# Kernel tuning notes

Hardware: AMD Instinct MI355X
Metric: run time of the kernel (lower is better)

The kernel has to match this reference:

```python
import jax, jax.numpy as jnp
import numpy as np

B, C, H, W = 8, 512, 32, 32
NUM_HEADS = 8
HEAD_DIM = C // NUM_HEADS
SCALE = 1.0 / float(np.sqrt(HEAD_DIM))


def setup_inputs() -> dict:
    key = jax.random.key(0)
    ks = jax.random.split(key, 6)
    x = jax.random.normal(ks[0], (B, C, H, W), dtype=jnp.float32)
    attn_mask = jax.random.randint(ks[1], (B, H, W), 0, 2).astype(jnp.bool_)
    # 1x1 conv weights are equivalent to channel matmuls: (out_ch, in_ch)
    w_std = 1.0 / float(np.sqrt(C))
    qkv_w = jax.random.uniform(ks[2], (3 * C, C), jnp.float32, -w_std, w_std)
    qkv_b = jax.random.uniform(ks[3], (3 * C,), jnp.float32, -w_std, w_std)
    proj_w = jax.random.uniform(ks[4], (C, C), jnp.float32, -w_std, w_std)
    proj_b = jax.random.uniform(ks[5], (C,), jnp.float32, -w_std, w_std)
    return {"x": x, "attn_mask": attn_mask, "qkv_w": qkv_w, "qkv_b": qkv_b,
            "proj_w": proj_w, "proj_b": proj_b}


def reference(x, attn_mask, qkv_w, qkv_b, proj_w, proj_b):
    b, c, h, w = x.shape
    S = h * w
    neg = jnp.finfo(x.dtype).min
    # qkv 1x1 conv: (B,3C,H,W)
    qkv = jnp.einsum('oc,bchw->bohw', qkv_w, x) + qkv_b[None, :, None, None]
    q, k, v = jnp.split(qkv, 3, axis=1)

    def split_heads(z):
        # (B, C, H, W) -> (B, heads, head_dim, S)
        return z.reshape(b, NUM_HEADS, HEAD_DIM, S)

    q, k, v = split_heads(q), split_heads(k), split_heads(v)
    # scores[s,t] = sum_d q[d,s] * k[d,t]
    scores = jnp.einsum('bhds,bhdt->bhst', q, k) * SCALE
    idx = jnp.arange(S)
    causal = (idx[None, :] > idx[:, None])[None, None]  # (1,1,S,S), True above diag
    scores = jnp.where(causal, neg, scores)
    kpm = attn_mask.reshape(b, 1, 1, S)  # key padding mask, True = mask out
    scores = jnp.where(kpm, neg, scores)
    attn = jax.nn.softmax(scores, axis=-1)
    # ctx[d,s] = sum_t v[d,t] * attn[s,t]
    ctx = jnp.einsum('bhdt,bhst->bhds', v, attn)
    ctx = ctx.reshape(b, c, h, w)
    out = jnp.einsum('oc,bchw->bohw', proj_w, ctx) + proj_b[None, :, None, None]
    return out
```

## Files before the change

kernel.cpp:

```cpp
#include <hip/hip_runtime.h>
#include <cfloat>
#include <math.h>

#define SB 1024
#define CC 512
#define NB 8
#define NH 8
#define HD 64

typedef short short8 __attribute__((ext_vector_type(8)));
typedef short s16x4 __attribute__((ext_vector_type(4)));
typedef float f32x4 __attribute__((ext_vector_type(4)));

__device__ __forceinline__ short f2bs(float f) {
    union { float f; unsigned u; } x; x.f = f;
    unsigned r = x.u + 0x7fffu + ((x.u >> 16) & 1u);
    return (short)(r >> 16);
}

__device__ __forceinline__ float bs2f(short s) {
    union { unsigned u; float f; } x;
    x.u = ((unsigned)(unsigned short)s) << 16;
    return x.f;
}

__device__ __forceinline__ void gload16(const void* g, void* l) {
    __builtin_amdgcn_global_load_lds(
        (const __attribute__((address_space(1))) unsigned int*)g,
        (__attribute__((address_space(3))) unsigned int*)l, 16, 0, 0);
}

__device__ __forceinline__ int sidx(int row, int colb) {
    return row * 64 + ((colb ^ ((row & 7) << 4)) >> 1);
}

__global__ __launch_bounds__(256)
void cvt_weights(const float* __restrict__ w1, const float* __restrict__ w2,
                 short* __restrict__ o1, short* __restrict__ o2)
{
    const int i4 = blockIdx.x * 256 + threadIdx.x;
    const int N1 = 1536 * 512 / 4;
    if (i4 < N1) {
        float4 v = *(const float4*)&w1[(size_t)i4 * 4];
        s16x4 p; p[0] = f2bs(v.x); p[1] = f2bs(v.y); p[2] = f2bs(v.z); p[3] = f2bs(v.w);
        *(s16x4*)&o1[(size_t)i4 * 4] = p;
    } else {
        const int j = i4 - N1;
        float4 v = *(const float4*)&w2[(size_t)j * 4];
        s16x4 p; p[0] = f2bs(v.x); p[1] = f2bs(v.y); p[2] = f2bs(v.z); p[3] = f2bs(v.w);
        *(s16x4*)&o2[(size_t)j * 4] = p;
    }
}

__global__ __launch_bounds__(256)
void transpose_x(const float* __restrict__ x, short* __restrict__ xT)
{
    const int bs = blockIdx.x, bc = blockIdx.y, b = blockIdx.z;
    const int tid = threadIdx.x;
    __shared__ short T[64][72];
    {
        const int cl = tid >> 4;
        const int s4 = (tid & 15) * 4;
        #pragma unroll
        for (int r = 0; r < 4; ++r) {
            const int c = cl + 16 * r;
            float4 v = *(const float4*)&x[((size_t)b * CC + bc * 64 + c) * SB + bs * 64 + s4];
            T[s4 + 0][c] = f2bs(v.x); T[s4 + 1][c] = f2bs(v.y);
            T[s4 + 2][c] = f2bs(v.z); T[s4 + 3][c] = f2bs(v.w);
        }
    }
    __syncthreads();
    {
        const int sl = tid >> 2;
        const int c16 = (tid & 3) * 16;
        short8 v0 = *(const short8*)&T[sl][c16];
        short8 v1 = *(const short8*)&T[sl][c16 + 8];
        short* dst = &xT[((size_t)b * SB + bs * 64 + sl) * CC + bc * 64 + c16];
        *(short8*)&dst[0] = v0;
        *(short8*)&dst[8] = v1;
    }
}

__global__ __launch_bounds__(256)
void vmean_kernel(const short* __restrict__ vN, const int* __restrict__ mask,
                  float* __restrict__ vmean, float* __restrict__ maskf)
{
    const int gi = blockIdx.x * 256 + threadIdx.x;
    if (gi < NB * SB) maskf[gi] = (mask[gi] != 0) ? -FLT_MAX : 0.f;

    const int row = blockIdx.x * 4 + (threadIdx.x >> 6);
    const int lane = threadIdx.x & 63;
    const short* p = vN + (size_t)row * SB + lane * 16;
    short8 a = *(const short8*)&p[0];
    short8 b8 = *(const short8*)&p[8];
    float s = 0.f;
    #pragma unroll
    for (int j = 0; j < 8; ++j) s += bs2f(a[j]) + bs2f(b8[j]);
    #pragma unroll
    for (int o = 1; o < 64; o <<= 1) s += __shfl_xor(s, o, 64);
    if (lane == 0) vmean[row] = s * (1.f / 1024.f);
}

template<int MODE>
__global__ __launch_bounds__(256)
void gemm_bf16(const short* __restrict__ A, const float* __restrict__ bias,
               const short* __restrict__ BT,
               short* __restrict__ qTo, short* __restrict__ kTo,
               short* __restrict__ vo, float* __restrict__ fo)
{
    const int stile = blockIdx.x * 128;
    const int bo    = blockIdx.y;
    const int b     = blockIdx.z;
    const int tid   = threadIdx.x;
    const int wave = tid >> 6, lane = tid & 63, lg = lane >> 4, ln = lane & 15;
    const int wm = wave >> 1, wn = wave & 1;

    __shared__ short Al[128 * 64];
    __shared__ short Bl[128 * 64];

    f32x4 acc[4][4];
    #pragma unroll
    for (int mt = 0; mt < 4; ++mt)
        #pragma unroll
        for (int nt = 0; nt < 4; ++nt) acc[mt][nt] = (f32x4){0.f, 0.f, 0.f, 0.f};

    const char* Ab = (const char*)(A + (size_t)bo * 128 * 512);
    const char* Bb = (const char*)(BT + ((size_t)b * SB + stile) * 512);

    for (int kc = 0; kc < 512; kc += 64) {
        __syncthreads();
        #pragma unroll
        for (int sw = 0; sw < 4; ++sw) {
            const int lin = tid * 16 + sw * 4096;
            const int row = lin >> 7;
            const int scol = (lin & 127) ^ ((row & 7) << 4);
            gload16(Ab + ((size_t)row * 512 + kc) * 2 + scol,
                    (char*)Al + (wave << 10) + (sw << 12));
            gload16(Bb + ((size_t)row * 512 + kc) * 2 + scol,
                    (char*)Bl + (wave << 10) + (sw << 12));
        }
        __syncthreads();
        #pragma unroll
        for (int kk = 0; kk < 2; ++kk) {
            const int colb = kk * 64 + lg * 16;
            short8 a[4], bb[4];
            #pragma unroll
            for (int mt = 0; mt < 4; ++mt)
                a[mt] = *(const short8*)&Al[sidx(wm * 64 + mt * 16 + ln, colb)];
            #pragma unroll
            for (int nt = 0; nt < 4; ++nt)
                bb[nt] = *(const short8*)&Bl[sidx(wn * 64 + nt * 16 + ln, colb)];
            #pragma unroll
            for (int mt = 0; mt < 4; ++mt)
                #pragma unroll
                for (int nt = 0; nt < 4; ++nt)
                    acc[mt][nt] = __builtin_amdgcn_mfma_f32_16x16x32_bf16(
                        a[mt], bb[nt], acc[mt][nt], 0, 0, 0);
        }
    }

    const int s_base = stile + wn * 64;
    if (MODE == 0) {
        if (bo < 8) {
            short* dst = (bo < 4) ? qTo : kTo;
            const int h = (bo & 3) * 2 + wm;
            const float sc = (bo < 4) ? 0.18033688011112042f : 1.0f;
            #pragma unroll
            for (int mt = 0; mt < 4; ++mt) {
                const int d0 = mt * 16 + 4 * lg;
                const int o0 = bo * 128 + wm * 64 + d0;
                const float b0 = bias[o0], b1 = bias[o0 + 1],
                            b2 = bias[o0 + 2], b3 = bias[o0 + 3];
                #pragma unroll
                for (int nt = 0; nt < 4; ++nt) {
                    const int s = s_base + nt * 16 + ln;
                    s16x4 pk;
                    pk[0] = f2bs((acc[mt][nt][0] + b0) * sc);
                    pk[1] = f2bs((acc[mt][nt][1] + b1) * sc);
                    pk[2] = f2bs((acc[mt][nt][2] + b2) * sc);
                    pk[3] = f2bs((acc[mt][nt][3] + b3) * sc);
                    *(s16x4*)&dst[(((size_t)b * NH + h) * SB + s) * HD + d0] = pk;
                }
            }
        } else {
            #pragma unroll
            for (int mt = 0; mt < 4; ++mt) {
                const int cv0 = (bo - 8) * 128 + wm * 64 + mt * 16 + 4 * lg;
                #pragma unroll
                for (int r = 0; r < 4; ++r) {
                    const float bv = bias[1024 + cv0 + r];
                    #pragma unroll
                    for (int nt = 0; nt < 4; ++nt) {
                        const int s = s_base + nt * 16 + ln;
                        vo[((size_t)b * CC + cv0 + r) * SB + s] = f2bs(acc[mt][nt][r] + bv);
                    }
                }
            }
        }
    } else {
        #pragma unroll
        for (int mt = 0; mt < 4; ++mt) {
            #pragma unroll
            for (int r = 0; r < 4; ++r) {
                const int o = bo * 128 + wm * 64 + mt * 16 + 4 * lg + r;
                const float bv = bias[o];
                #pragma unroll
                for (int nt = 0; nt < 4; ++nt) {
                    const int s = s_base + nt * 16 + ln;
                    fo[((size_t)b * CC + o) * SB + s] = acc[mt][nt][r] + bv;
                }
            }
        }
    }
}

__global__ __launch_bounds__(256, 4)
void attn_mfma(const short* __restrict__ qT, const short* __restrict__ kT,
               const short* __restrict__ vN, const float* __restrict__ maskf,
               const float* __restrict__ vmean, short* __restrict__ ctxT)
{
    const int L  = blockIdx.x;
    const int qb = 15 - (L >> 6);
    const int bh = L & 63;
    const int b  = bh >> 3, h = bh & 7;
    const int tid = threadIdx.x;
    const int wave = tid >> 6;
    const int lane = tid & 63;
    const int lg = lane >> 4;
    const int ln = lane & 15;

    __shared__ short Ks[2][64 * 64];
    __shared__ short Vs[2][64 * 64];
    __shared__ float mskL[2][64];
    __shared__ short Ps[4][16][72];

    const char*  kbh = (const char*)(kT + (((size_t)b * NH + h) * SB) * HD);
    const char*  vbh = (const char*)(vN + ((size_t)b * CC + h * HD) * SB);
    const float* mb  = maskf + (size_t)b * SB;

    short8 qa0, qa1;
    {
        const short* qrow = qT + (((size_t)b * NH + h) * SB + qb * 64 + wave * 16 + ln) * HD;
        qa0 = *(const short8*)&qrow[8 * lg];
        qa1 = *(const short8*)&qrow[32 + 8 * lg];
    }

    float m_ = -FLT_MAX, l_ = 0.f;
    f32x4 acc[4];
    #pragma unroll
    for (int nt = 0; nt < 4; ++nt) acc[nt] = (f32x4){0.f, 0.f, 0.f, 0.f};

    auto stage = [&](int tb, int bi) {
        #pragma unroll
        for (int sw = 0; sw < 2; ++sw) {
            const int lin = tid * 16 + sw * 4096;
            const int row = lin >> 7;
            const int scol = (lin & 127) ^ ((row & 7) << 4);
            gload16(kbh + (size_t)tb * 128 + row * 128 + scol,
                    (char*)&Ks[bi][0] + (wave << 10) + (sw << 12));
            gload16(vbh + (size_t)row * (SB * 2) + tb * 2 + scol,
                    (char*)&Vs[bi][0] + (wave << 10) + (sw << 12));
        }
        if (tid < 64) mskL[bi][tid] = mb[tb + tid];
    };

    int cur = 0;
    stage(0, 0);
    __syncthreads();

    for (int t = 0; t <= qb; ++t) {
        if (t < qb) stage((t + 1) * 64, cur ^ 1);

        f32x4 sc[4];
        #pragma unroll
        for (int nt = 0; nt < 4; ++nt) {
            short8 kb0 = *(const short8*)&Ks[cur][sidx(ln + 16 * nt, lg * 16)];
            short8 kb1 = *(const short8*)&Ks[cur][sidx(ln + 16 * nt, 64 + lg * 16)];
            f32x4 z = (f32x4){0.f, 0.f, 0.f, 0.f};
            z = __builtin_amdgcn_mfma_f32_16x16x32_bf16(kb0, qa0, z, 0, 0, 0);
            z = __builtin_amdgcn_mfma_f32_16x16x32_bf16(kb1, qa1, z, 0, 0, 0);
            sc[nt] = z;
        }

        #pragma unroll
        for (int nt = 0; nt < 4; ++nt) {
            const float4 mf = *(const float4*)&mskL[cur][16 * nt + 4 * lg];
            sc[nt][0] += mf.x; sc[nt][1] += mf.y;
            sc[nt][2] += mf.z; sc[nt][3] += mf.w;
        }
        if (t == qb) {
            const int so = wave * 16 + ln;
            #pragma unroll
            for (int nt = 0; nt < 4; ++nt)
                #pragma unroll
                for (int r = 0; r < 4; ++r)
                    if (16 * nt + 4 * lg + r > so) sc[nt][r] = -FLT_MAX;
        }

        float mx = sc[0][0];
        #pragma unroll
        for (int nt = 0; nt < 4; ++nt)
            #pragma unroll
            for (int r = 0; r < 4; ++r)
                if (nt | r) mx = fmaxf(mx, sc[nt][r]);
        mx = fmaxf(mx, __shfl_xor(mx, 16, 64));
        mx = fmaxf(mx, __shfl_xor(mx, 32, 64));

        if (!__all(mx <= m_ + 11.5f)) {
            const float mnew = fmaxf(m_, mx);
            const float fq = exp2f(m_ - mnew);
            l_ *= fq;
            #pragma unroll
            for (int nt = 0; nt < 4; ++nt)
                #pragma unroll
                for (int r = 0; r < 4; ++r) acc[nt][r] *= fq;
            m_ = mnew;
        }

        float rs = 0.f;
        #pragma unroll
        for (int nt = 0; nt < 4; ++nt) {
            s16x4 pk;
            #pragma unroll
            for (int r = 0; r < 4; ++r) {
                const float p = exp2f(sc[nt][r] - m_);
                rs += p;
                pk[r] = f2bs(p);
            }
            *(s16x4*)&Ps[wave][ln][16 * nt + 4 * lg] = pk;
        }
        rs += __shfl_xor(rs, 16, 64);
        rs += __shfl_xor(rs, 32, 64);
        l_ += rs;

        const short8 pa0 = *(const short8*)&Ps[wave][ln][8 * lg];
        const short8 pa1 = *(const short8*)&Ps[wave][ln][32 + 8 * lg];
        #pragma unroll
        for (int nt = 0; nt < 4; ++nt) {
            short8 va0 = *(const short8*)&Vs[cur][sidx(16 * nt + ln, lg * 16)];
            short8 va1 = *(const short8*)&Vs[cur][sidx(16 * nt + ln, 64 + lg * 16)];
            acc[nt] = __builtin_amdgcn_mfma_f32_16x16x32_bf16(va0, pa0, acc[nt], 0, 0, 0);
            acc[nt] = __builtin_amdgcn_mfma_f32_16x16x32_bf16(va1, pa1, acc[nt], 0, 0, 0);
        }

        if (t < qb) {
            __syncthreads();
            cur ^= 1;
        }
    }

    const float rl = 1.f / l_;
    const bool dead = (m_ == -FLT_MAX);
    const float* vmb = vmean + (size_t)b * CC + h * HD;
    const int s = qb * 64 + wave * 16 + ln;
    short* crow = ctxT + ((size_t)b * SB + s) * CC + h * HD;
    #pragma unroll
    for (int nt = 0; nt < 4; ++nt) {
        const int d0 = 16 * nt + 4 * lg;
        const float4 vm4 = *(const float4*)&vmb[d0];
        s16x4 pk;
        pk[0] = f2bs(dead ? vm4.x : acc[nt][0] * rl);
        pk[1] = f2bs(dead ? vm4.y : acc[nt][1] * rl);
        pk[2] = f2bs(dead ? vm4.z : acc[nt][2] * rl);
        pk[3] = f2bs(dead ? vm4.w : acc[nt][3] * rl);
        *(s16x4*)&crow[d0] = pk;
    }
}

extern "C" void kernel_launch(void* const* d_in, const int* in_sizes, int n_in,
                              void* d_out, int out_size, void* d_ws, size_t ws_size,
                              hipStream_t stream) {
    const float* x      = (const float*)d_in[0];
    const int*   amask  = (const int*)d_in[1];
    const float* qkv_w  = (const float*)d_in[2];
    const float* qkv_b  = (const float*)d_in[3];
    const float* proj_w = (const float*)d_in[4];
    const float* proj_b = (const float*)d_in[5];
    float* out = (float*)d_out;

    short* xT    = (short*)d_ws;
    short* w1b   = xT  + (size_t)NB * SB * CC;
    short* w2b   = w1b + (size_t)1536 * 512;
    short* qT    = w2b + (size_t)512 * 512;
    short* kT    = qT  + (size_t)NB * NH * SB * HD;
    short* vN    = kT  + (size_t)NB * NH * SB * HD;
    short* ctxT  = vN  + (size_t)NB * CC * SB;
    float* vmean = (float*)(ctxT + (size_t)NB * SB * CC);
    float* maskf = vmean + (size_t)NB * CC;

    cvt_weights<<<1024, 256, 0, stream>>>(qkv_w, proj_w, w1b, w2b);
    transpose_x<<<dim3(SB / 64, CC / 64, NB), 256, 0, stream>>>(x, xT);
    gemm_bf16<0><<<dim3(8, 12, NB), 256, 0, stream>>>(
        w1b, qkv_b, xT, qT, kT, vN, nullptr);
    vmean_kernel<<<NB * CC / 4, 256, 0, stream>>>(vN, amask, vmean, maskf);
    attn_mfma<<<dim3(1024, 1, 1), 256, 0, stream>>>(qT, kT, vN, maskf, vmean, ctxT);
    gemm_bf16<1><<<dim3(8, 4, NB), 256, 0, stream>>>(
        w2b, proj_b, ctxT, nullptr, nullptr, nullptr, out);
}
```

Before: 85.14 us.

## Merge prep kernels, fuse V mean into QKV GEMM, pair causal query blocks

Merges weight conversion, x transpose, mask conversion and vmean zeroing into one prep launch. Computes the V row means inside the QKV GEMM epilogue with shuffles and atomics, which removes the separate vmean kernel. The attention kernel now gives each block two query tiles (qb and 15-qb) that share the K/V tiles, so causal work is even across 512 blocks and K/V loads are reused. In exchange it uses more registers and LDS, lowers the occupancy hint to 3, and adds float atomics whose summation order is not deterministic.

```diff
diff --git a/kernel.cpp b/kernel.cpp
--- a/kernel.cpp
+++ b/kernel.cpp
@@ -18,12 +18,6 @@
     return (short)(r >> 16);
 }
 
-__device__ __forceinline__ float bs2f(short s) {
-    union { unsigned u; float f; } x;
-    x.u = ((unsigned)(unsigned short)s) << 16;
-    return x.f;
-}
-
 __device__ __forceinline__ void gload16(const void* g, void* l) {
     __builtin_amdgcn_global_load_lds(
         (const __attribute__((address_space(1))) unsigned int*)g,
@@ -35,70 +29,59 @@
 }
 
 __global__ __launch_bounds__(256)
-void cvt_weights(const float* __restrict__ w1, const float* __restrict__ w2,
-                 short* __restrict__ o1, short* __restrict__ o2)
+void prep(const float* __restrict__ w1, const float* __restrict__ w2,
+          short* __restrict__ o1, short* __restrict__ o2,
+          const float* __restrict__ x, short* __restrict__ xT,
+          const int* __restrict__ mask, float* __restrict__ maskf,
+          float* __restrict__ vmean)
 {
-    const int i4 = blockIdx.x * 256 + threadIdx.x;
-    const int N1 = 1536 * 512 / 4;
-    if (i4 < N1) {
-        float4 v = *(const float4*)&w1[(size_t)i4 * 4];
-        s16x4 p; p[0] = f2bs(v.x); p[1] = f2bs(v.y); p[2] = f2bs(v.z); p[3] = f2bs(v.w);
-        *(s16x4*)&o1[(size_t)i4 * 4] = p;
+    const int B = blockIdx.x;
+    const int tid = threadIdx.x;
+    if (B < 1024) {
+        const int i4 = B * 256 + tid;
+        const int N1 = 1536 * 512 / 4;
+        if (i4 < N1) {
+            float4 v = *(const float4*)&w1[(size_t)i4 * 4];
+            s16x4 p; p[0] = f2bs(v.x); p[1] = f2bs(v.y); p[2] = f2bs(v.z); p[3] = f2bs(v.w);
+            *(s16x4*)&o1[(size_t)i4 * 4] = p;
+        } else {
+            const int j = i4 - N1;
+            float4 v = *(const float4*)&w2[(size_t)j * 4];
+            s16x4 p; p[0] = f2bs(v.x); p[1] = f2bs(v.y); p[2] = f2bs(v.z); p[3] = f2bs(v.w);
+            *(s16x4*)&o2[(size_t)j * 4] = p;
+        }
+    } else if (B < 2048) {
+        const int idx = B - 1024;
+        const int bs = idx & 15, bc = (idx >> 4) & 7, b = idx >> 7;
+        __shared__ short T[64][72];
+        {
+            const int cl = tid >> 4;
+            const int s4 = (tid & 15) * 4;
+            #pragma unroll
+            for (int r = 0; r < 4; ++r) {
+                const int c = cl + 16 * r;
+                float4 v = *(const float4*)&x[((size_t)b * CC + bc * 64 + c) * SB + bs * 64 + s4];
+                T[s4 + 0][c] = f2bs(v.x); T[s4 + 1][c] = f2bs(v.y);
+                T[s4 + 2][c] = f2bs(v.z); T[s4 + 3][c] = f2bs(v.w);
+            }
+        }
+        __syncthreads();
+        {
+            const int sl = tid >> 2;
+            const int c16 = (tid & 3) * 16;
+            short8 v0 = *(const short8*)&T[sl][c16];
+            short8 v1 = *(const short8*)&T[sl][c16 + 8];
+            short* dst = &xT[((size_t)b * SB + bs * 64 + sl) * CC + bc * 64 + c16];
+            *(short8*)&dst[0] = v0;
+            *(short8*)&dst[8] = v1;
+        }
+    } else if (B < 2080) {
+        const int gi = (B - 2048) * 256 + tid;
+        if (gi < NB * SB) maskf[gi] = (mask[gi] != 0) ? -FLT_MAX : 0.f;
     } else {
-        const int j = i4 - N1;
-        float4 v = *(const float4*)&w2[(size_t)j * 4];
-        s16x4 p; p[0] = f2bs(v.x); p[1] = f2bs(v.y); p[2] = f2bs(v.z); p[3] = f2bs(v.w);
-        *(s16x4*)&o2[(size_t)j * 4] = p;
-    }
-}
-
-__global__ __launch_bounds__(256)
-void transpose_x(const float* __restrict__ x, short* __restrict__ xT)
-{
-    const int bs = blockIdx.x, bc = blockIdx.y, b = blockIdx.z;
-    const int tid = threadIdx.x;
-    __shared__ short T[64][72];
-    {
-        const int cl = tid >> 4;
-        const int s4 = (tid & 15) * 4;
-        #pragma unroll
-        for (int r = 0; r < 4; ++r) {
-            const int c = cl + 16 * r;
-            float4 v = *(const float4*)&x[((size_t)b * CC + bc * 64 + c) * SB + bs * 64 + s4];
-            T[s4 + 0][c] = f2bs(v.x); T[s4 + 1][c] = f2bs(v.y);
-            T[s4 + 2][c] = f2bs(v.z); T[s4 + 3][c] = f2bs(v.w);
-        }
-    }
-    __syncthreads();
-    {
-        const int sl = tid >> 2;
-        const int c16 = (tid & 3) * 16;
-        short8 v0 = *(const short8*)&T[sl][c16];
-        short8 v1 = *(const short8*)&T[sl][c16 + 8];
-        short* dst = &xT[((size_t)b * SB + bs * 64 + sl) * CC + bc * 64 + c16];
-        *(short8*)&dst[0] = v0;
-        *(short8*)&dst[8] = v1;
-    }
-}
-
-__global__ __launch_bounds__(256)
-void vmean_kernel(const short* __restrict__ vN, const int* __restrict__ mask,
-                  float* __restrict__ vmean, float* __restrict__ maskf)
-{
-    const int gi = blockIdx.x * 256 + threadIdx.x;
-    if (gi < NB * SB) maskf[gi] = (mask[gi] != 0) ? -FLT_MAX : 0.f;
-
-    const int row = blockIdx.x * 4 + (threadIdx.x >> 6);
-    const int lane = threadIdx.x & 63;
-    const short* p = vN + (size_t)row * SB + lane * 16;
-    short8 a = *(const short8*)&p[0];
-    short8 b8 = *(const short8*)&p[8];
-    float s = 0.f;
-    #pragma unroll
-    for (int j = 0; j < 8; ++j) s += bs2f(a[j]) + bs2f(b8[j]);
-    #pragma unroll
-    for (int o = 1; o < 64; o <<= 1) s += __shfl_xor(s, o, 64);
-    if (lane == 0) vmean[row] = s * (1.f / 1024.f);
+        const int i = (B - 2080) * 256 + tid;
+        if (i < NB * CC) vmean[i] = 0.f;
+    }
 }
 
 template<int MODE>
@@ -106,7 +89,8 @@
 void gemm_bf16(const short* __restrict__ A, const float* __restrict__ bias,
                const short* __restrict__ BT,
                short* __restrict__ qTo, short* __restrict__ kTo,
-               short* __restrict__ vo, float* __restrict__ fo)
+               short* __restrict__ vo, float* __restrict__ fo,
+               float* __restrict__ vmean)
 {
     const int stile = blockIdx.x * 128;
     const int bo    = blockIdx.y;
@@ -189,11 +173,19 @@
                 #pragma unroll
                 for (int r = 0; r < 4; ++r) {
                     const float bv = bias[1024 + cv0 + r];
+                    float part = 0.f;
                     #pragma unroll
                     for (int nt = 0; nt < 4; ++nt) {
                         const int s = s_base + nt * 16 + ln;
-                        vo[((size_t)b * CC + cv0 + r) * SB + s] = f2bs(acc[mt][nt][r] + bv);
+                        const float val = acc[mt][nt][r] + bv;
+                        part += val;
+                        vo[((size_t)b * CC + cv0 + r) * SB + s] = f2bs(val);
                     }
+                    #pragma unroll
+                    for (int o = 1; o < 16; o <<= 1)
+                        part += __shfl_xor(part, o, 64);
+                    if (ln == 0)
+                        atomicAdd(&vmean[(size_t)b * CC + cv0 + r], part);
                 }
             }
         }
@@ -214,14 +206,15 @@
     }
 }
 
-__global__ __launch_bounds__(256, 4)
+__global__ __launch_bounds__(256, 3)
 void attn_mfma(const short* __restrict__ qT, const short* __restrict__ kT,
                const short* __restrict__ vN, const float* __restrict__ maskf,
                const float* __restrict__ vmean, short* __restrict__ ctxT)
 {
     const int L  = blockIdx.x;
-    const int qb = 15 - (L >> 6);
+    const int pa = L >> 6;
     const int bh = L & 63;
+    const int qbA = pa, qbB = 15 - pa;
     const int b  = bh >> 3, h = bh & 7;
     const int tid = threadIdx.x;
     const int wave = tid >> 6;
@@ -232,23 +225,29 @@
     __shared__ short Ks[2][64 * 64];
     __shared__ short Vs[2][64 * 64];
     __shared__ float mskL[2][64];
-    __shared__ short Ps[4][16][72];
+    __shared__ short Ps[4][2][16][72];
 
     const char*  kbh = (const char*)(kT + (((size_t)b * NH + h) * SB) * HD);
     const char*  vbh = (const char*)(vN + ((size_t)b * CC + h * HD) * SB);
     const float* mb  = maskf + (size_t)b * SB;
 
-    short8 qa0, qa1;
+    short8 qaA0, qaA1, qaB0, qaB1;
     {
-        const short* qrow = qT + (((size_t)b * NH + h) * SB + qb * 64 + wave * 16 + ln) * HD;
-        qa0 = *(const short8*)&qrow[8 * lg];
-        qa1 = *(const short8*)&qrow[32 + 8 * lg];
-    }
-
-    float m_ = -FLT_MAX, l_ = 0.f;
-    f32x4 acc[4];
+        const short* qra = qT + (((size_t)b * NH + h) * SB + qbA * 64 + wave * 16 + ln) * HD;
+        qaA0 = *(const short8*)&qra[8 * lg];
+        qaA1 = *(const short8*)&qra[32 + 8 * lg];
+        const short* qrb = qT + (((size_t)b * NH + h) * SB + qbB * 64 + wave * 16 + ln) * HD;
+        qaB0 = *(const short8*)&qrb[8 * lg];
+        qaB1 = *(const short8*)&qrb[32 + 8 * lg];
+    }
+
+    float mA = -FLT_MAX, lA = 0.f, mB = -FLT_MAX, lB = 0.f;
+    f32x4 accA[4], accB[4];
     #pragma unroll
-    for (int nt = 0; nt < 4; ++nt) acc[nt] = (f32x4){0.f, 0.f, 0.f, 0.f};
+    for (int nt = 0; nt < 4; ++nt) {
+        accA[nt] = (f32x4){0.f, 0.f, 0.f, 0.f};
+        accB[nt] = (f32x4){0.f, 0.f, 0.f, 0.f};
+    }
 
     auto stage = [&](int tb, int bi) {
         #pragma unroll
@@ -268,102 +267,181 @@
     stage(0, 0);
     __syncthreads();
 
-    for (int t = 0; t <= qb; ++t) {
-        if (t < qb) stage((t + 1) * 64, cur ^ 1);
-
-        f32x4 sc[4];
+    for (int t = 0; t <= qbB; ++t) {
+        if (t < qbB) stage((t + 1) * 64, cur ^ 1);
+        const bool doA = (t <= qbA);
+
+        f32x4 scA[4], scB[4];
         #pragma unroll
         for (int nt = 0; nt < 4; ++nt) {
             short8 kb0 = *(const short8*)&Ks[cur][sidx(ln + 16 * nt, lg * 16)];
             short8 kb1 = *(const short8*)&Ks[cur][sidx(ln + 16 * nt, 64 + lg * 16)];
-            f32x4 z = (f32x4){0.f, 0.f, 0.f, 0.f};
-            z = __builtin_amdgcn_mfma_f32_16x16x32_bf16(kb0, qa0, z, 0, 0, 0);
-            z = __builtin_amdgcn_mfma_f32_16x16x32_bf16(kb1, qa1, z, 0, 0, 0);
-            sc[nt] = z;
+            f32x4 zb = (f32x4){0.f, 0.f, 0.f, 0.f};
+            zb = __builtin_amdgcn_mfma_f32_16x16x32_bf16(kb0, qaB0, zb, 0, 0, 0);
+            zb = __builtin_amdgcn_mfma_f32_16x16x32_bf16(kb1, qaB1, zb, 0, 0, 0);
+            scB[nt] = zb;
+            if (doA) {
+                f32x4 za = (f32x4){0.f, 0.f, 0.f, 0.f};
+                za = __builtin_amdgcn_mfma_f32_16x16x32_bf16(kb0, qaA0, za, 0, 0, 0);
+                za = __builtin_amdgcn_mfma_f32_16x16x32_bf16(kb1, qaA1, za, 0, 0, 0);
+                scA[nt] = za;
+            }
         }
 
         #pragma unroll
         for (int nt = 0; nt < 4; ++nt) {
             const float4 mf = *(const float4*)&mskL[cur][16 * nt + 4 * lg];
-            sc[nt][0] += mf.x; sc[nt][1] += mf.y;
-            sc[nt][2] += mf.z; sc[nt][3] += mf.w;
-        }
-        if (t == qb) {
-            const int so = wave * 16 + ln;
+            scB[nt][0] += mf.x; scB[nt][1] += mf.y;
+            scB[nt][2] += mf.z; scB[nt][3] += mf.w;
+            if (doA) {
+                scA[nt][0] += mf.x; scA[nt][1] += mf.y;
+                scA[nt][2] += mf.z; scA[nt][3] += mf.w;
+            }
+        }
+        const int so = wave * 16 + ln;
+        if (t == qbA) {
             #pragma unroll
             for (int nt = 0; nt < 4; ++nt)
                 #pragma unroll
                 for (int r = 0; r < 4; ++r)
-                    if (16 * nt + 4 * lg + r > so) sc[nt][r] = -FLT_MAX;
-        }
-
-        float mx = sc[0][0];
-        #pragma unroll
-        for (int nt = 0; nt < 4; ++nt)
-            #pragma unroll
-            for (int r = 0; r < 4; ++r)
-                if (nt | r) mx = fmaxf(mx, sc[nt][r]);
-        mx = fmaxf(mx, __shfl_xor(mx, 16, 64));
-        mx = fmaxf(mx, __shfl_xor(mx, 32, 64));
-
-        if (!__all(mx <= m_ + 11.5f)) {
-            const float mnew = fmaxf(m_, mx);
-            const float fq = exp2f(m_ - mnew);
-            l_ *= fq;
+                    if (16 * nt + 4 * lg + r > so) scA[nt][r] = -FLT_MAX;
+        }
+        if (t == qbB) {
             #pragma unroll
             for (int nt = 0; nt < 4; ++nt)
                 #pragma unroll
-                for (int r = 0; r < 4; ++r) acc[nt][r] *= fq;
-            m_ = mnew;
-        }
-
-        float rs = 0.f;
-        #pragma unroll
-        for (int nt = 0; nt < 4; ++nt) {
-            s16x4 pk;
-            #pragma unroll
-            for (int r = 0; r < 4; ++r) {
-                const float p = exp2f(sc[nt][r] - m_);
-                rs += p;
-                pk[r] = f2bs(p);
-            }
-            *(s16x4*)&Ps[wave][ln][16 * nt + 4 * lg] = pk;
-        }
-        rs += __shfl_xor(rs, 16, 64);
-        rs += __shfl_xor(rs, 32, 64);
-        l_ += rs;
-
-        const short8 pa0 = *(const short8*)&Ps[wave][ln][8 * lg];
-        const short8 pa1 = *(const short8*)&Ps[wave][ln][32 + 8 * lg];
+                for (int r = 0; r < 4; ++r)
+                    if (16 * nt + 4 * lg + r > so) scB[nt][r] = -FLT_MAX;
+        }
+
+        if (doA) {
+            float mx = scA[0][0];
+            #pragma unroll
+            for (int nt = 0; nt < 4; ++nt)
+                #pragma unroll
+                for (int r = 0; r < 4; ++r)
+                    if (nt | r) mx = fmaxf(mx, scA[nt][r]);
+            mx = fmaxf(mx, __shfl_xor(mx, 16, 64));
+            mx = fmaxf(mx, __shfl_xor(mx, 32, 64));
+            if (!__all(mx <= mA + 11.5f)) {
+                const float mnew = fmaxf(mA, mx);
+                const float fq = exp2f(mA - mnew);
+                lA *= fq;
+                #pragma unroll
+                for (int nt = 0; nt < 4; ++nt)
+                    #pragma unroll
+                    for (int r = 0; r < 4; ++r) accA[nt][r] *= fq;
+                mA = mnew;
+            }
+            float rs = 0.f;
+            #pragma unroll
+            for (int nt = 0; nt < 4; ++nt) {
+                s16x4 pk;
+                #pragma unroll
+                for (int r = 0; r < 4; ++r) {
+                    const float p = exp2f(scA[nt][r] - mA);
+                    rs += p;
+                    pk[r] = f2bs(p);
+                }
+                *(s16x4*)&Ps[wave][0][ln][16 * nt + 4 * lg] = pk;
+            }
+            rs += __shfl_xor(rs, 16, 64);
+            rs += __shfl_xor(rs, 32, 64);
+            lA += rs;
+        }
+
+        {
+            float mx = scB[0][0];
+            #pragma unroll
+            for (int nt = 0; nt < 4; ++nt)
+                #pragma unroll
+                for (int r = 0; r < 4; ++r)
+                    if (nt | r) mx = fmaxf(mx, scB[nt][r]);
+            mx = fmaxf(mx, __shfl_xor(mx, 16, 64));
+            mx = fmaxf(mx, __shfl_xor(mx, 32, 64));
+            if (!__all(mx <= mB + 11.5f)) {
+                const float mnew = fmaxf(mB, mx);
+                const float fq = exp2f(mB - mnew);
+                lB *= fq;
+                #pragma unroll
+                for (int nt = 0; nt < 4; ++nt)
+                    #pragma unroll
+                    for (int r = 0; r < 4; ++r) accB[nt][r] *= fq;
+                mB = mnew;
+            }
+            float rs = 0.f;
+            #pragma unroll
+            for (int nt = 0; nt < 4; ++nt) {
+                s16x4 pk;
+                #pragma unroll
+                for (int r = 0; r < 4; ++r) {
+                    const float p = exp2f(scB[nt][r] - mB);
+                    rs += p;
+                    pk[r] = f2bs(p);
+                }
+                *(s16x4*)&Ps[wave][1][ln][16 * nt + 4 * lg] = pk;
+            }
+            rs += __shfl_xor(rs, 16, 64);
+            rs += __shfl_xor(rs, 32, 64);
+            lB += rs;
+        }
+
+        const short8 paA0 = *(const short8*)&Ps[wave][0][ln][8 * lg];
+        const short8 paA1 = *(const short8*)&Ps[wave][0][ln][32 + 8 * lg];
+        const short8 paB0 = *(const short8*)&Ps[wave][1][ln][8 * lg];
+        const short8 paB1 = *(const short8*)&Ps[wave][1][ln][32 + 8 * lg];
         #pragma unroll
         for (int nt = 0; nt < 4; ++nt) {
             short8 va0 = *(const short8*)&Vs[cur][sidx(16 * nt + ln, lg * 16)];
             short8 va1 = *(const short8*)&Vs[cur][sidx(16 * nt + ln, 64 + lg * 16)];
-            acc[nt] = __builtin_amdgcn_mfma_f32_16x16x32_bf16(va0, pa0, acc[nt], 0, 0, 0);
-            acc[nt] = __builtin_amdgcn_mfma_f32_16x16x32_bf16(va1, pa1, acc[nt], 0, 0, 0);
-        }
-
-        if (t < qb) {
+            accB[nt] = __builtin_amdgcn_mfma_f32_16x16x32_bf16(va0, paB0, accB[nt], 0, 0, 0);
+            accB[nt] = __builtin_amdgcn_mfma_f32_16x16x32_bf16(va1, paB1, accB[nt], 0, 0, 0);
+            if (doA) {
+                accA[nt] = __builtin_amdgcn_mfma_f32_16x16x32_bf16(va0, paA0, accA[nt], 0, 0, 0);
+                accA[nt] = __builtin_amdgcn_mfma_f32_16x16x32_bf16(va1, paA1, accA[nt], 0, 0, 0);
+            }
+        }
+
+        if (t < qbB) {
             __syncthreads();
             cur ^= 1;
         }
     }
 
-    const float rl = 1.f / l_;
-    const bool dead = (m_ == -FLT_MAX);
     const float* vmb = vmean + (size_t)b * CC + h * HD;
-    const int s = qb * 64 + wave * 16 + ln;
-    short* crow = ctxT + ((size_t)b * SB + s) * CC + h * HD;
-    #pragma unroll
-    for (int nt = 0; nt < 4; ++nt) {
-        const int d0 = 16 * nt + 4 * lg;
-        const float4 vm4 = *(const float4*)&vmb[d0];
-        s16x4 pk;
-        pk[0] = f2bs(dead ? vm4.x : acc[nt][0] * rl);
-        pk[1] = f2bs(dead ? vm4.y : acc[nt][1] * rl);
-        pk[2] = f2bs(dead ? vm4.z : acc[nt][2] * rl);
-        pk[3] = f2bs(dead ? vm4.w : acc[nt][3] * rl);
-        *(s16x4*)&crow[d0] = pk;
+    {
+        const float rl = 1.f / lA;
+        const bool dead = (mA == -FLT_MAX);
+        const int s = qbA * 64 + wave * 16 + ln;
+        short* crow = ctxT + ((size_t)b * SB + s) * CC + h * HD;
+        #pragma unroll
+        for (int nt = 0; nt < 4; ++nt) {
+            const int d0 = 16 * nt + 4 * lg;
+            const float4 vm4 = *(const float4*)&vmb[d0];
+            s16x4 pk;
+            pk[0] = f2bs(dead ? vm4.x * (1.f / 1024.f) : accA[nt][0] * rl);
+            pk[1] = f2bs(dead ? vm4.y * (1.f / 1024.f) : accA[nt][1] * rl);
+            pk[2] = f2bs(dead ? vm4.z * (1.f / 1024.f) : accA[nt][2] * rl);
+            pk[3] = f2bs(dead ? vm4.w * (1.f / 1024.f) : accA[nt][3] * rl);
+            *(s16x4*)&crow[d0] = pk;
+        }
+    }
+    {
+        const float rl = 1.f / lB;
+        const bool dead = (mB == -FLT_MAX);
+        const int s = qbB * 64 + wave * 16 + ln;
+        short* crow = ctxT + ((size_t)b * SB + s) * CC + h * HD;
+        #pragma unroll
+        for (int nt = 0; nt < 4; ++nt) {
+            const int d0 = 16 * nt + 4 * lg;
+            const float4 vm4 = *(const float4*)&vmb[d0];
+            s16x4 pk;
+            pk[0] = f2bs(dead ? vm4.x * (1.f / 1024.f) : accB[nt][0] * rl);
+            pk[1] = f2bs(dead ? vm4.y * (1.f / 1024.f) : accB[nt][1] * rl);
+            pk[2] = f2bs(dead ? vm4.z * (1.f / 1024.f) : accB[nt][2] * rl);
+            pk[3] = f2bs(dead ? vm4.w * (1.f / 1024.f) : accB[nt][3] * rl);
+            *(s16x4*)&crow[d0] = pk;
+        }
     }
 }
 
@@ -388,12 +466,11 @@
     float* vmean = (float*)(ctxT + (size_t)NB * SB * CC);
     float* maskf = vmean + (size_t)NB * CC;
 
-    cvt_weights<<<1024, 256, 0, stream>>>(qkv_w, proj_w, w1b, w2b);
-    transpose_x<<<dim3(SB / 64, CC / 64, NB), 256, 0, stream>>>(x, xT);
+    prep<<<2096, 256, 0, stream>>>(qkv_w, proj_w, w1b, w2b, x, xT,
+                                   amask, maskf, vmean);
     gemm_bf16<0><<<dim3(8, 12, NB), 256, 0, stream>>>(
-        w1b, qkv_b, xT, qT, kT, vN, nullptr);
-    vmean_kernel<<<NB * CC / 4, 256, 0, stream>>>(vN, amask, vmean, maskf);
-    attn_mfma<<<dim3(1024, 1, 1), 256, 0, stream>>>(qT, kT, vN, maskf, vmean, ctxT);
+        w1b, qkv_b, xT, qT, kT, vN, nullptr, vmean);
+    attn_mfma<<<dim3(512, 1, 1), 256, 0, stream>>>(qT, kT, vN, maskf, vmean, ctxT);
     gemm_bf16<1><<<dim3(8, 4, NB), 256, 0, stream>>>(
-        w2b, proj_b, ctxT, nullptr, nullptr, nullptr, out);
-}
+        w2b, proj_b, ctxT, nullptr, nullptr, nullptr, out, nullptr);
+}
```

New measurement: 86.67 us. Within noise of the previous version (+1.8%).
